# Kernel optimization log

Measured on AMD Instinct MI355X. Metric: run time of the kernel, lower is better.

The kernel has to match this reference:

```python
import jax, jax.numpy as jnp
import numpy as np

LAMB_MAX = 2.0


def cheb_conv_k2(x, edge_index, w0, w1, b):
    """PyG ChebConv with K=2, sym normalization, given lambda_max.
    out = x @ w0 + (L_hat x) @ w1 + b, where
    L_hat = (2/lmax) * (I - D^{-1/2} A D^{-1/2}) - I.
    """
    n = x.shape[0]
    src, dst = edge_index[0], edge_index[1]
    ew = jnp.ones(src.shape, x.dtype)
    deg = jax.ops.segment_sum(ew, src, num_segments=n)
    dinv = jnp.where(deg > 0, jax.lax.rsqrt(jnp.maximum(deg, 1e-12)), 0.0)
    s = 2.0 / LAMB_MAX
    # off-diagonal weights of scaled Laplacian: -s * d_i^{-1/2} d_j^{-1/2}
    norm = (-s) * dinv[src] * dinv[dst]  # [E]
    # gather-scale-scatter: (L_hat x)_offdiag
    agg = jax.ops.segment_sum(norm[:, None] * x[src], dst, num_segments=n)  # [N, F]
    tx1 = (s - 1.0) * x + agg  # diagonal: s*1 (L diag) + (-1) self-loop
    return x @ w0 + tx1 @ w1 + b


def setup_inputs() -> dict:
    key = jax.random.key(0)
    ks = jax.random.split(key, 8)
    N, E, F, H = 100000, 1600000, 128, 128
    x = jax.random.normal(ks[0], (N, F), dtype=jnp.float32)
    edge_index = jax.random.randint(ks[1], (2, E), 0, N, dtype=jnp.int32)
    # glorot-ish init for the two Chebyshev linear weights per layer
    sc1 = (2.0 / (F + H)) ** 0.5
    sc2 = (2.0 / (H + 1)) ** 0.5
    w1_0 = jax.random.normal(ks[2], (F, H), dtype=jnp.float32) * sc1
    w1_1 = jax.random.normal(ks[3], (F, H), dtype=jnp.float32) * sc1
    b1 = jnp.zeros((H,), jnp.float32)
    w2_0 = jax.random.normal(ks[4], (H, 1), dtype=jnp.float32) * sc2
    w2_1 = jax.random.normal(ks[5], (H, 1), dtype=jnp.float32) * sc2
    b2 = jnp.zeros((1,), jnp.float32)
    return {"x": x, "edge_index": edge_index, "w1_0": w1_0, "w1_1": w1_1,
            "b1": b1, "w2_0": w2_0, "w2_1": w2_1, "b2": b2}


def reference(x, edge_index, w1_0, w1_1, b1, w2_0, w2_1, b2):
    h = jax.nn.relu(cheb_conv_k2(x, edge_index, w1_0, w1_1, b1))
    out = jax.nn.sigmoid(cheb_conv_k2(h, edge_index, w2_0, w2_1, b2))
    return out  # [N, 1]
```

## Files before the change

### kernel.cpp

```cpp
#include <hip/hip_runtime.h>
#include <math.h>

#define F 128
#define SCAN_CHUNK 1024
#define CHUNK 32
#define NBLK 128

typedef __attribute__((ext_vector_type(8))) short bf16x8;
typedef __attribute__((ext_vector_type(4))) float f32x4;

__device__ inline unsigned short f2bf(float v) {
  unsigned u = __float_as_uint(v);
  unsigned r = (u + 0x7FFFu + ((u >> 16) & 1u)) >> 16;
  return (unsigned short)r;
}
__device__ inline float bf2f(unsigned short s) {
  return __uint_as_float(((unsigned)s) << 16);
}

__global__ __launch_bounds__(1024) void k_prep2(const int* __restrict__ src,
                                                const int* __restrict__ dst,
                                                const float* __restrict__ x,
                                                unsigned short* __restrict__ xb,
                                                int* __restrict__ cntgD,
                                                int* __restrict__ cntgS, int E,
                                                int NF4, int nb, int per) {
  extern __shared__ int smem[];
  int* cd = smem;
  int* cs = smem + nb;
  int blk = blockIdx.x;
  int tid = threadIdx.x;
  for (int b = tid; b < nb; b += 1024) {
    cd[b] = 0;
    cs[b] = 0;
  }
  __syncthreads();
  int e0 = blk * per;
  int e1 = e0 + per;
  if (e1 > E) e1 = E;
  for (int e = e0 + tid; e < e1; e += 1024) {
    atomicAdd(&cd[dst[e] >> 7], 1);
    atomicAdd(&cs[src[e] >> 7], 1);
  }
  const float4* x4 = (const float4*)x;
  ushort4* xb4 = (ushort4*)xb;
  for (int i = blk * 1024 + tid; i < NF4; i += NBLK * 1024) {
    float4 v = x4[i];
    ushort4 o;
    o.x = f2bf(v.x);
    o.y = f2bf(v.y);
    o.z = f2bf(v.z);
    o.w = f2bf(v.w);
    xb4[i] = o;
  }
  __syncthreads();
  for (int b = tid; b < nb; b += 1024) {
    cntgD[b * NBLK + blk] = cd[b];
    cntgS[b * NBLK + blk] = cs[b];
  }
}

__global__ __launch_bounds__(NBLK) void k_scanBk2(int* __restrict__ cntgD,
                                                  int* __restrict__ cntgS,
                                                  int* __restrict__ totD,
                                                  int* __restrict__ totS, int nb) {
  __shared__ int sh[NBLK];
  int b = blockIdx.x;
  int tid = threadIdx.x;
  int* cntg;
  int* tot;
  int bb;
  if (b < nb) {
    cntg = cntgD;
    tot = totD;
    bb = b;
  } else {
    cntg = cntgS;
    tot = totS;
    bb = b - nb;
  }
  int v = cntg[bb * NBLK + tid];
  int val = v;
  sh[tid] = val;
  __syncthreads();
  for (int off = 1; off < NBLK; off <<= 1) {
    int o = (tid >= off) ? sh[tid - off] : 0;
    __syncthreads();
    val += o;
    sh[tid] = val;
    __syncthreads();
  }
  cntg[bb * NBLK + tid] = val - v;
  if (tid == NBLK - 1) tot[bb] = val;
}

__global__ __launch_bounds__(1024) void k_scanTot(const int* __restrict__ totD,
                                                  const int* __restrict__ totS,
                                                  int* __restrict__ baseD,
                                                  int* __restrict__ baseS, int nb,
                                                  int E) {
  __shared__ int sh[1024];
  int tid = threadIdx.x;
  int v = (tid < nb) ? totD[tid] : 0;
  int val = v;
  sh[tid] = val;
  __syncthreads();
  for (int off = 1; off < 1024; off <<= 1) {
    int o = (tid >= off) ? sh[tid - off] : 0;
    __syncthreads();
    val += o;
    sh[tid] = val;
    __syncthreads();
  }
  if (tid < nb) baseD[tid] = val - v;
  if (tid == 0) baseD[nb] = E;
  __syncthreads();
  v = (tid < nb) ? totS[tid] : 0;
  val = v;
  sh[tid] = val;
  __syncthreads();
  for (int off = 1; off < 1024; off <<= 1) {
    int o = (tid >= off) ? sh[tid - off] : 0;
    __syncthreads();
    val += o;
    sh[tid] = val;
    __syncthreads();
  }
  if (tid < nb) baseS[tid] = val - v;
  if (tid == 0) baseS[nb] = E;
}

__global__ __launch_bounds__(1024) void k_binfill2(
    const int* __restrict__ src, const int* __restrict__ dst,
    const int* __restrict__ cntgD, const int* __restrict__ cntgS,
    const int* __restrict__ baseD, const int* __restrict__ baseS,
    unsigned* __restrict__ binnedD, unsigned char* __restrict__ binnedS, int E,
    int nb, int per) {
  extern __shared__ int smem[];
  int* bD = smem;
  int* cD = smem + nb;
  int* bS = smem + 2 * nb;
  int* cS = smem + 3 * nb;
  int blk = blockIdx.x;
  for (int b = threadIdx.x; b < nb; b += 1024) {
    bD[b] = baseD[b] + cntgD[b * NBLK + blk];
    cD[b] = 0;
    bS[b] = baseS[b] + cntgS[b * NBLK + blk];
    cS[b] = 0;
  }
  __syncthreads();
  int e0 = blk * per;
  int e1 = e0 + per;
  if (e1 > E) e1 = E;
  for (int e = e0 + threadIdx.x; e < e1; e += 1024) {
    int s = src[e];
    int d = dst[e];
    int bk = d >> 7;
    int rk = atomicAdd(&cD[bk], 1);
    binnedD[bD[bk] + rk] = ((unsigned)s << 7) | (unsigned)(d & 127);
    int bs = s >> 7;
    int rs = atomicAdd(&cS[bs], 1);
    binnedS[bS[bs] + rs] = (unsigned char)(s & 127);
  }
}

__global__ __launch_bounds__(256) void k_csr(const unsigned char* __restrict__ binnedS,
                                             const int* __restrict__ baseS,
                                             const unsigned* __restrict__ binnedD,
                                             const int* __restrict__ baseD,
                                             float* __restrict__ dinv,
                                             int* __restrict__ rp,
                                             int* __restrict__ pairs, int N, int E) {
  __shared__ int cnt[128];
  __shared__ int sc[256];
  __shared__ int cur[128];
  int b = blockIdx.x;
  int tid = threadIdx.x;
  int node0 = b << 7;
  if (tid < 128) cnt[tid] = 0;
  __syncthreads();
  int sbeg = baseS[b], send = baseS[b + 1];
  for (int j = sbeg + tid; j < send; j += 256) atomicAdd(&cnt[binnedS[j]], 1);
  __syncthreads();
  if (tid < 128) {
    int node = node0 + tid;
    if (node < N) {
      int c = cnt[tid];
      dinv[node] = c > 0 ? rsqrtf((float)c) : 0.0f;
    }
    cnt[tid] = 0;
  }
  __syncthreads();
  int wbeg = baseD[b], wend = baseD[b + 1];
  for (int j = wbeg + tid; j < wend; j += 256) atomicAdd(&cnt[binnedD[j] & 127u], 1);
  __syncthreads();
  int v = (tid < 128) ? cnt[tid] : 0;
  int val = v;
  sc[tid] = val;
  __syncthreads();
  for (int off = 1; off < 128; off <<= 1) {
    int o = (tid >= off) ? sc[tid - off] : 0;
    __syncthreads();
    val += o;
    sc[tid] = val;
    __syncthreads();
  }
  if (tid < 128) {
    int excl = wbeg + val - v;
    int node = node0 + tid;
    if (node < N) rp[node] = excl;
    cur[tid] = excl;
  }
  if (b == 0 && tid == 0) rp[N] = E;
  __syncthreads();
  for (int j = wbeg + tid; j < wend; j += 256) {
    unsigned e = binnedD[j];
    int idx = atomicAdd(&cur[e & 127u], 1);
    pairs[idx] = (int)(e >> 7);
  }
}

__global__ __launch_bounds__(256) void k_prep(const int* __restrict__ src,
                                              const int* __restrict__ dst,
                                              const float* __restrict__ x,
                                              int* __restrict__ degA,
                                              int* __restrict__ degB,
                                              unsigned short* __restrict__ xb,
                                              int E, int NF4) {
  int t0 = blockIdx.x * 256 + threadIdx.x;
  int stride = gridDim.x * 256;
  for (int i = t0; i < E; i += stride) {
    atomicAdd(&degA[src[i]], 1);
    atomicAdd(&degB[dst[i]], 1);
  }
  const float4* x4 = (const float4*)x;
  ushort4* xb4 = (ushort4*)xb;
  for (int i = t0; i < NF4; i += stride) {
    float4 v = x4[i];
    ushort4 o;
    o.x = f2bf(v.x);
    o.y = f2bf(v.y);
    o.z = f2bf(v.z);
    o.w = f2bf(v.w);
    xb4[i] = o;
  }
}

__global__ __launch_bounds__(256) void k_scanA(const int* __restrict__ deg,
                                               int* __restrict__ rp,
                                               int* __restrict__ bsum, int N) {
  __shared__ int sh[256];
  int tid = threadIdx.x;
  int base = blockIdx.x * SCAN_CHUNK + tid * 4;
  int v0 = 0, v1 = 0, v2 = 0, v3 = 0;
  if (base + 0 < N) v0 = deg[base + 0];
  if (base + 1 < N) v1 = deg[base + 1];
  if (base + 2 < N) v2 = deg[base + 2];
  if (base + 3 < N) v3 = deg[base + 3];
  int ts = v0 + v1 + v2 + v3;
  int val = ts;
  sh[tid] = val;
  __syncthreads();
  for (int off = 1; off < 256; off <<= 1) {
    int other = (tid >= off) ? sh[tid - off] : 0;
    __syncthreads();
    val += other;
    sh[tid] = val;
    __syncthreads();
  }
  int excl = val - ts;
  if (base + 0 < N) rp[base + 0] = excl;
  if (base + 1 < N) rp[base + 1] = excl + v0;
  if (base + 2 < N) rp[base + 2] = excl + v0 + v1;
  if (base + 3 < N) rp[base + 3] = excl + v0 + v1 + v2;
  if (tid == 255) bsum[blockIdx.x] = val;
}

__global__ __launch_bounds__(256) void k_scanB(int* __restrict__ bsum, int nb) {
  __shared__ int sh[256];
  int tid = threadIdx.x;
  int ts = (tid < nb) ? bsum[tid] : 0;
  int val = ts;
  sh[tid] = val;
  __syncthreads();
  for (int off = 1; off < 256; off <<= 1) {
    int other = (tid >= off) ? sh[tid - off] : 0;
    __syncthreads();
    val += other;
    sh[tid] = val;
    __syncthreads();
  }
  if (tid < nb) bsum[tid] = val - ts;
}

__global__ __launch_bounds__(256) void k_scanC(int* __restrict__ rp,
                                               const int* __restrict__ bsum,
                                               int* __restrict__ pos,
                                               const int* __restrict__ degA,
                                               float* __restrict__ dinv, int N,
                                               int E) {
  int i = blockIdx.x * 256 + threadIdx.x;
  if (i < N) {
    int v = rp[i] + bsum[i >> 10];
    rp[i] = v;
    pos[i] = v;
    int d = degA[i];
    dinv[i] = d > 0 ? rsqrtf((float)d) : 0.0f;
  }
  if (i == 0) rp[N] = E;
}

__global__ __launch_bounds__(256) void k_fill(const int* __restrict__ src,
                                              const int* __restrict__ dst,
                                              int* __restrict__ pos,
                                              int* __restrict__ pairs, int E) {
  for (int e = blockIdx.x * 256 + threadIdx.x; e < E; e += gridDim.x * 256) {
    int s = src[e];
    int d = dst[e];
    int idx = atomicAdd(&pos[d], 1);
    pairs[idx] = s;
  }
}

__global__ __launch_bounds__(256) void k_gather1c(
    const int* __restrict__ pairs, const int* __restrict__ rp,
    const unsigned short* __restrict__ xb, const float* __restrict__ dinv,
    unsigned short* __restrict__ tb, int N) {
  int node = (blockIdx.x * 256 + threadIdx.x) >> 5;
  if (node >= N) return;
  int li = threadIdx.x & 31;
  int beg = rp[node], end = rp[node + 1];
  const uint2* x2 = (const uint2*)xb;
  float a0 = 0.f, a1 = 0.f, a2 = 0.f, a3 = 0.f;
  int j = beg;
  for (; j + 3 < end; j += 4) {
    int s0 = pairs[j], s1 = pairs[j + 1], s2 = pairs[j + 2], s3 = pairs[j + 3];
    float w0 = dinv[s0], w1 = dinv[s1], w2 = dinv[s2], w3 = dinv[s3];
    uint2 v0 = x2[(size_t)s0 * 32 + li];
    uint2 v1 = x2[(size_t)s1 * 32 + li];
    uint2 v2 = x2[(size_t)s2 * 32 + li];
    uint2 v3 = x2[(size_t)s3 * 32 + li];
    a0 += w0 * bf2f((unsigned short)v0.x) + w1 * bf2f((unsigned short)v1.x) +
          w2 * bf2f((unsigned short)v2.x) + w3 * bf2f((unsigned short)v3.x);
    a1 += w0 * bf2f((unsigned short)(v0.x >> 16)) +
          w1 * bf2f((unsigned short)(v1.x >> 16)) +
          w2 * bf2f((unsigned short)(v2.x >> 16)) +
          w3 * bf2f((unsigned short)(v3.x >> 16));
    a2 += w0 * bf2f((unsigned short)v0.y) + w1 * bf2f((unsigned short)v1.y) +
          w2 * bf2f((unsigned short)v2.y) + w3 * bf2f((unsigned short)v3.y);
    a3 += w0 * bf2f((unsigned short)(v0.y >> 16)) +
          w1 * bf2f((unsigned short)(v1.y >> 16)) +
          w2 * bf2f((unsigned short)(v2.y >> 16)) +
          w3 * bf2f((unsigned short)(v3.y >> 16));
  }
  for (; j < end; ++j) {
    int s0 = pairs[j];
    float w0 = dinv[s0];
    uint2 v0 = x2[(size_t)s0 * 32 + li];
    a0 += w0 * bf2f((unsigned short)v0.x);
    a1 += w0 * bf2f((unsigned short)(v0.x >> 16));
    a2 += w0 * bf2f((unsigned short)v0.y);
    a3 += w0 * bf2f((unsigned short)(v0.y >> 16));
  }
  float nd = -dinv[node];
  uint2 o;
  o.x = ((unsigned)f2bf(nd * a1) << 16) | f2bf(nd * a0);
  o.y = ((unsigned)f2bf(nd * a3) << 16) | f2bf(nd * a2);
  ((uint2*)tb)[(size_t)node * 32 + li] = o;
}

__global__ __launch_bounds__(256) void k_layer_mfma(
    const unsigned short* __restrict__ xb, const unsigned short* __restrict__ tb,
    const float* __restrict__ dinv, const float* __restrict__ w10,
    const float* __restrict__ w11, const float* __restrict__ b1,
    const float* __restrict__ w20, const float* __restrict__ w21,
    float* __restrict__ p, float* __restrict__ r, int N) {
  __shared__ __align__(16) short Ax[8 * 16 * 40];
  __shared__ __align__(16) short At[8 * 16 * 40];
  __shared__ float p_sh[CHUNK], r_sh[CHUNK];

  const int tid = threadIdx.x;
  const int wave = tid >> 6;
  const int lane = tid & 63;
  const int quad = lane >> 4;
  const int col = lane & 15;

  bf16x8 Bh[2][4][2], Bl[2][4][2];
  float b1f[2], w20f[2], w21f[2];
#pragma unroll
  for (int nt = 0; nt < 2; ++nt) {
    int f = wave * 32 + nt * 16 + col;
    b1f[nt] = b1[f];
    w20f[nt] = w20[f];
    w21f[nt] = w21[f];
  }
#pragma unroll
  for (int mat = 0; mat < 2; ++mat) {
    const float* w = mat ? w11 : w10;
#pragma unroll
    for (int ks = 0; ks < 4; ++ks) {
#pragma unroll
      for (int nt = 0; nt < 2; ++nt) {
        int f = wave * 32 + nt * 16 + col;
        bf16x8 h8, l8;
#pragma unroll
        for (int j = 0; j < 8; ++j) {
          float v = w[(ks * 32 + quad * 8 + j) * F + f];
          unsigned short hi = f2bf(v);
          l8[j] = (short)f2bf(v - bf2f(hi));
          h8[j] = (short)hi;
        }
        Bh[mat][ks][nt] = h8;
        Bl[mat][ks][nt] = l8;
      }
    }
  }

  const int nchunks = (N + CHUNK - 1) / CHUNK;
  for (int chunk = blockIdx.x; chunk < nchunks; chunk += gridDim.x) {
    int node0 = chunk * CHUNK;
    __syncthreads();

    {
      int nloc = tid >> 3;
      int k0 = (tid & 7) * 16;
      int gn = node0 + nloc;
      int mt = nloc >> 4, m = nloc & 15, ks = k0 >> 5, koff = k0 & 31;
      int base = ((mt * 4 + ks) * 16 + m) * 40 + koff;
      const uint2* xr = (const uint2*)(xb + (size_t)gn * F + k0);
      const uint2* tr = (const uint2*)(tb + (size_t)gn * F + k0);
      bool ok = (gn < N);
#pragma unroll
      for (int q4 = 0; q4 < 4; ++q4) {
        uint2 xv = ok ? xr[q4] : make_uint2(0u, 0u);
        uint2 tv = ok ? tr[q4] : make_uint2(0u, 0u);
        *(uint2*)&Ax[base + q4 * 4] = xv;
        *(uint2*)&At[base + q4 * 4] = tv;
      }
      if (tid < CHUNK) {
        p_sh[tid] = 0.f;
        r_sh[tid] = 0.f;
      }
    }
    __syncthreads();

    f32x4 acc[2][2];
#pragma unroll
    for (int mt = 0; mt < 2; ++mt)
#pragma unroll
      for (int nt = 0; nt < 2; ++nt) acc[mt][nt] = (f32x4)0.f;

#pragma unroll
    for (int mt = 0; mt < 2; ++mt) {
#pragma unroll
      for (int ks = 0; ks < 4; ++ks) {
        int ab = ((mt * 4 + ks) * 16 + col) * 40 + quad * 8;
        bf16x8 ax = *(bf16x8*)&Ax[ab];
        bf16x8 at = *(bf16x8*)&At[ab];
#pragma unroll
        for (int nt = 0; nt < 2; ++nt) {
          f32x4 c = acc[mt][nt];
          c = __builtin_amdgcn_mfma_f32_16x16x32_bf16(ax, Bh[0][ks][nt], c, 0, 0, 0);
          c = __builtin_amdgcn_mfma_f32_16x16x32_bf16(ax, Bl[0][ks][nt], c, 0, 0, 0);
          c = __builtin_amdgcn_mfma_f32_16x16x32_bf16(at, Bh[1][ks][nt], c, 0, 0, 0);
          c = __builtin_amdgcn_mfma_f32_16x16x32_bf16(at, Bl[1][ks][nt], c, 0, 0, 0);
          acc[mt][nt] = c;
        }
      }
    }

#pragma unroll
    for (int mt = 0; mt < 2; ++mt) {
      float pp[4], rr[4];
#pragma unroll
      for (int reg = 0; reg < 4; ++reg) {
        float h0 = fmaxf(acc[mt][0][reg] + b1f[0], 0.f);
        float h1 = fmaxf(acc[mt][1][reg] + b1f[1], 0.f);
        pp[reg] = h0 * w20f[0] + h1 * w20f[1];
        rr[reg] = h0 * w21f[0] + h1 * w21f[1];
      }
#pragma unroll
      for (int off = 1; off < 16; off <<= 1) {
#pragma unroll
        for (int reg = 0; reg < 4; ++reg) {
          pp[reg] += __shfl_xor(pp[reg], off);
          rr[reg] += __shfl_xor(rr[reg], off);
        }
      }
      if (col == 0) {
#pragma unroll
        for (int reg = 0; reg < 4; ++reg) {
          atomicAdd(&p_sh[mt * 16 + quad * 4 + reg], pp[reg]);
          atomicAdd(&r_sh[mt * 16 + quad * 4 + reg], rr[reg]);
        }
      }
    }
    __syncthreads();
    if (tid < CHUNK) {
      int gn = node0 + tid;
      if (gn < N) {
        p[gn] = p_sh[tid];
        r[gn] = dinv[gn] * r_sh[tid];
      }
    }
  }
}

__global__ __launch_bounds__(256) void k_gather2_final(
    const int* __restrict__ pairs, const int* __restrict__ rp,
    const float* __restrict__ r2, const float* __restrict__ p,
    const float* __restrict__ dinv, const float* __restrict__ b2,
    float* __restrict__ out, int N) {
  int i = blockIdx.x * 256 + threadIdx.x;
  if (i >= N) return;
  int beg = rp[i], end = rp[i + 1];
  float a = 0.f;
  for (int j = beg; j < end; ++j) a += r2[pairs[j]];
  float z = p[i] - dinv[i] * a + b2[0];
  out[i] = 1.0f / (1.0f + expf(-z));
}

extern "C" void kernel_launch(void* const* d_in, const int* in_sizes, int n_in,
                              void* d_out, int out_size, void* d_ws, size_t ws_size,
                              hipStream_t stream) {
  const float* x = (const float*)d_in[0];
  const int* ei = (const int*)d_in[1];
  const float* w10 = (const float*)d_in[2];
  const float* w11 = (const float*)d_in[3];
  const float* b1 = (const float*)d_in[4];
  const float* w20 = (const float*)d_in[5];
  const float* w21 = (const float*)d_in[6];
  const float* b2 = (const float*)d_in[7];
  float* out = (float*)d_out;
  int N = in_sizes[0] / F;
  int E = in_sizes[1] / 2;
  const int* src = ei;
  const int* dst = ei + E;
  int nbuckets = (N + 127) >> 7;

  size_t off = 0;
  char* base = (char*)d_ws;
  auto take = [&](size_t bytes) {
    void* ptr = base + off;
    off += (bytes + 15) & ~(size_t)15;
    return ptr;
  };
  float* dinv = (float*)take((size_t)N * 4);
  float* p = (float*)take((size_t)N * 4);
  float* r = (float*)take((size_t)N * 4);
  int* rp = (int*)take(((size_t)N + 1) * 4);
  int* degA = (int*)take((size_t)N * 4);
  int* degB = (int*)take((size_t)N * 4);
  int* pos = (int*)take((size_t)N * 4);
  int* bsum = (int*)take(256 * 4);
  int* cntgD = (int*)take((size_t)nbuckets * NBLK * 4);
  int* cntgS = (int*)take((size_t)nbuckets * NBLK * 4);
  int* totD = (int*)take(((size_t)nbuckets + 1) * 4);
  int* totS = (int*)take(((size_t)nbuckets + 1) * 4);
  int* baseD = (int*)take(((size_t)nbuckets + 1) * 4);
  int* baseS = (int*)take(((size_t)nbuckets + 1) * 4);
  int* pairs = (int*)take((size_t)E * 4);
  unsigned short* xb = (unsigned short*)take((size_t)N * F * 2);
  unsigned short* tb = (unsigned short*)take((size_t)N * F * 2);
  if (off > ws_size) return;
  unsigned* binnedD = (unsigned*)tb;
  unsigned char* binnedS = (unsigned char*)tb + (((size_t)E * 4 + 255) & ~(size_t)255);

  int NF4 = N * (F / 4);
  int per = (E + NBLK - 1) / NBLK;

  if (nbuckets <= 1024 && (size_t)E * 5 + 256 <= (size_t)N * F * 2) {
    k_prep2<<<NBLK, 1024, (size_t)nbuckets * 8, stream>>>(src, dst, x, xb, cntgD,
                                                          cntgS, E, NF4, nbuckets,
                                                          per);
    k_scanBk2<<<2 * nbuckets, NBLK, 0, stream>>>(cntgD, cntgS, totD, totS, nbuckets);
    k_scanTot<<<1, 1024, 0, stream>>>(totD, totS, baseD, baseS, nbuckets, E);
    k_binfill2<<<NBLK, 1024, (size_t)nbuckets * 16, stream>>>(
        src, dst, cntgD, cntgS, baseD, baseS, binnedD, binnedS, E, nbuckets, per);
    k_csr<<<nbuckets, 256, 0, stream>>>(binnedS, baseS, binnedD, baseD, dinv, rp,
                                        pairs, N, E);
  } else {
    int nb_scan = (N + SCAN_CHUNK - 1) / SCAN_CHUNK;
    hipMemsetAsync(degA, 0, 2 * (size_t)N * sizeof(int), stream);
    k_prep<<<2048, 256, 0, stream>>>(src, dst, x, degA, degB, xb, E, NF4);
    k_scanA<<<nb_scan, 256, 0, stream>>>(degB, rp, bsum, N);
    k_scanB<<<1, 256, 0, stream>>>(bsum, nb_scan);
    k_scanC<<<(N + 255) / 256, 256, 0, stream>>>(rp, bsum, pos, degA, dinv, N, E);
    k_fill<<<2048, 256, 0, stream>>>(src, dst, pos, pairs, E);
  }
  k_gather1c<<<(N + 7) / 8, 256, 0, stream>>>(pairs, rp, xb, dinv, tb, N);
  k_layer_mfma<<<512, 256, 0, stream>>>(xb, tb, dinv, w10, w11, b1, w20, w21, p, r,
                                        N);
  k_gather2_final<<<(N + 255) / 256, 256, 0, stream>>>(pairs, rp, r, p, dinv, b2,
                                                       out, N);
}
```

Baseline: 313.3 us.

## Fuse layer-1 gather into MFMA layer kernel and drop split-bf16 weight terms

The neighbor gather-aggregate now runs inside the MFMA layer kernel and writes straight into shared memory, so the bf16 intermediate tb no longer round-trips through global memory. The grid becomes one block per 32-node chunk instead of a persistent loop. The weights are also reduced from a hi+lo bf16 split to a single bf16 term, which halves the MFMA count but lowers weight precision. Per-block setup, including loading and converting the weights into registers, is now repeated for each of about 3125 blocks, and the binned scratch buffers get their own workspace space.

```diff
diff --git a/kernel.cpp b/kernel.cpp
--- a/kernel.cpp
+++ b/kernel.cpp
@@ -322,59 +322,13 @@
   }
 }
 
-__global__ __launch_bounds__(256) void k_gather1c(
+__global__ __launch_bounds__(256) void k_fused(
     const int* __restrict__ pairs, const int* __restrict__ rp,
     const unsigned short* __restrict__ xb, const float* __restrict__ dinv,
-    unsigned short* __restrict__ tb, int N) {
-  int node = (blockIdx.x * 256 + threadIdx.x) >> 5;
-  if (node >= N) return;
-  int li = threadIdx.x & 31;
-  int beg = rp[node], end = rp[node + 1];
-  const uint2* x2 = (const uint2*)xb;
-  float a0 = 0.f, a1 = 0.f, a2 = 0.f, a3 = 0.f;
-  int j = beg;
-  for (; j + 3 < end; j += 4) {
-    int s0 = pairs[j], s1 = pairs[j + 1], s2 = pairs[j + 2], s3 = pairs[j + 3];
-    float w0 = dinv[s0], w1 = dinv[s1], w2 = dinv[s2], w3 = dinv[s3];
-    uint2 v0 = x2[(size_t)s0 * 32 + li];
-    uint2 v1 = x2[(size_t)s1 * 32 + li];
-    uint2 v2 = x2[(size_t)s2 * 32 + li];
-    uint2 v3 = x2[(size_t)s3 * 32 + li];
-    a0 += w0 * bf2f((unsigned short)v0.x) + w1 * bf2f((unsigned short)v1.x) +
-          w2 * bf2f((unsigned short)v2.x) + w3 * bf2f((unsigned short)v3.x);
-    a1 += w0 * bf2f((unsigned short)(v0.x >> 16)) +
-          w1 * bf2f((unsigned short)(v1.x >> 16)) +
-          w2 * bf2f((unsigned short)(v2.x >> 16)) +
-          w3 * bf2f((unsigned short)(v3.x >> 16));
-    a2 += w0 * bf2f((unsigned short)v0.y) + w1 * bf2f((unsigned short)v1.y) +
-          w2 * bf2f((unsigned short)v2.y) + w3 * bf2f((unsigned short)v3.y);
-    a3 += w0 * bf2f((unsigned short)(v0.y >> 16)) +
-          w1 * bf2f((unsigned short)(v1.y >> 16)) +
-          w2 * bf2f((unsigned short)(v2.y >> 16)) +
-          w3 * bf2f((unsigned short)(v3.y >> 16));
-  }
-  for (; j < end; ++j) {
-    int s0 = pairs[j];
-    float w0 = dinv[s0];
-    uint2 v0 = x2[(size_t)s0 * 32 + li];
-    a0 += w0 * bf2f((unsigned short)v0.x);
-    a1 += w0 * bf2f((unsigned short)(v0.x >> 16));
-    a2 += w0 * bf2f((unsigned short)v0.y);
-    a3 += w0 * bf2f((unsigned short)(v0.y >> 16));
-  }
-  float nd = -dinv[node];
-  uint2 o;
-  o.x = ((unsigned)f2bf(nd * a1) << 16) | f2bf(nd * a0);
-  o.y = ((unsigned)f2bf(nd * a3) << 16) | f2bf(nd * a2);
-  ((uint2*)tb)[(size_t)node * 32 + li] = o;
-}
-
-__global__ __launch_bounds__(256) void k_layer_mfma(
-    const unsigned short* __restrict__ xb, const unsigned short* __restrict__ tb,
-    const float* __restrict__ dinv, const float* __restrict__ w10,
-    const float* __restrict__ w11, const float* __restrict__ b1,
-    const float* __restrict__ w20, const float* __restrict__ w21,
-    float* __restrict__ p, float* __restrict__ r, int N) {
+    const float* __restrict__ w10, const float* __restrict__ w11,
+    const float* __restrict__ b1, const float* __restrict__ w20,
+    const float* __restrict__ w21, float* __restrict__ p, float* __restrict__ r,
+    int N) {
   __shared__ __align__(16) short Ax[8 * 16 * 40];
   __shared__ __align__(16) short At[8 * 16 * 40];
   __shared__ float p_sh[CHUNK], r_sh[CHUNK];
@@ -385,7 +339,7 @@
   const int quad = lane >> 4;
   const int col = lane & 15;
 
-  bf16x8 Bh[2][4][2], Bl[2][4][2];
+  bf16x8 B0[4][2], B1[4][2];
   float b1f[2], w20f[2], w21f[2];
 #pragma unroll
   for (int nt = 0; nt < 2; ++nt) {
@@ -395,113 +349,154 @@
     w21f[nt] = w21[f];
   }
 #pragma unroll
-  for (int mat = 0; mat < 2; ++mat) {
-    const float* w = mat ? w11 : w10;
+  for (int ks = 0; ks < 4; ++ks) {
+#pragma unroll
+    for (int nt = 0; nt < 2; ++nt) {
+      int f = wave * 32 + nt * 16 + col;
+      bf16x8 h0, h1;
+#pragma unroll
+      for (int j = 0; j < 8; ++j) {
+        h0[j] = (short)f2bf(w10[(ks * 32 + quad * 8 + j) * F + f]);
+        h1[j] = (short)f2bf(w11[(ks * 32 + quad * 8 + j) * F + f]);
+      }
+      B0[ks][nt] = h0;
+      B1[ks][nt] = h1;
+    }
+  }
+
+  int node0 = blockIdx.x * CHUNK;
+
+  {
+    int nloc = tid >> 3;
+    int k0 = (tid & 7) * 16;
+    int gn = node0 + nloc;
+    int mt = nloc >> 4, m = nloc & 15, ks = k0 >> 5, koff = k0 & 31;
+    int base = ((mt * 4 + ks) * 16 + m) * 40 + koff;
+    const uint2* xr = (const uint2*)(xb + (size_t)gn * F + k0);
+    bool ok = (gn < N);
+#pragma unroll
+    for (int q4 = 0; q4 < 4; ++q4) {
+      uint2 xv = ok ? xr[q4] : make_uint2(0u, 0u);
+      *(uint2*)&Ax[base + q4 * 4] = xv;
+    }
+    if (tid < CHUNK) {
+      p_sh[tid] = 0.f;
+      r_sh[tid] = 0.f;
+    }
+  }
+
+  {
+    int hw = tid >> 5;
+    int li = tid & 31;
+    const uint2* x2 = (const uint2*)xb;
+    int ks = li >> 3, koff = (li & 7) * 4;
+#pragma unroll 1
+    for (int nn = 0; nn < 4; ++nn) {
+      int nloc = hw * 4 + nn;
+      int gn = node0 + nloc;
+      float a0 = 0.f, a1 = 0.f, a2 = 0.f, a3 = 0.f;
+      float nd = 0.f;
+      if (gn < N) {
+        int beg = rp[gn], end = rp[gn + 1];
+        int j = beg;
+        for (; j + 3 < end; j += 4) {
+          int s0 = pairs[j], s1 = pairs[j + 1], s2 = pairs[j + 2], s3 = pairs[j + 3];
+          float w0 = dinv[s0], w1 = dinv[s1], w2 = dinv[s2], w3 = dinv[s3];
+          uint2 v0 = x2[(size_t)s0 * 32 + li];
+          uint2 v1 = x2[(size_t)s1 * 32 + li];
+          uint2 v2 = x2[(size_t)s2 * 32 + li];
+          uint2 v3 = x2[(size_t)s3 * 32 + li];
+          a0 += w0 * bf2f((unsigned short)v0.x) + w1 * bf2f((unsigned short)v1.x) +
+                w2 * bf2f((unsigned short)v2.x) + w3 * bf2f((unsigned short)v3.x);
+          a1 += w0 * bf2f((unsigned short)(v0.x >> 16)) +
+                w1 * bf2f((unsigned short)(v1.x >> 16)) +
+                w2 * bf2f((unsigned short)(v2.x >> 16)) +
+                w3 * bf2f((unsigned short)(v3.x >> 16));
+          a2 += w0 * bf2f((unsigned short)v0.y) + w1 * bf2f((unsigned short)v1.y) +
+                w2 * bf2f((unsigned short)v2.y) + w3 * bf2f((unsigned short)v3.y);
+          a3 += w0 * bf2f((unsigned short)(v0.y >> 16)) +
+                w1 * bf2f((unsigned short)(v1.y >> 16)) +
+                w2 * bf2f((unsigned short)(v2.y >> 16)) +
+                w3 * bf2f((unsigned short)(v3.y >> 16));
+        }
+        for (; j < end; ++j) {
+          int s0 = pairs[j];
+          float w0 = dinv[s0];
+          uint2 v0 = x2[(size_t)s0 * 32 + li];
+          a0 += w0 * bf2f((unsigned short)v0.x);
+          a1 += w0 * bf2f((unsigned short)(v0.x >> 16));
+          a2 += w0 * bf2f((unsigned short)v0.y);
+          a3 += w0 * bf2f((unsigned short)(v0.y >> 16));
+        }
+        nd = -dinv[gn];
+      }
+      int mt = nloc >> 4, m = nloc & 15;
+      int base = ((mt * 4 + ks) * 16 + m) * 40 + koff;
+      short4 o;
+      o.x = (short)f2bf(nd * a0);
+      o.y = (short)f2bf(nd * a1);
+      o.z = (short)f2bf(nd * a2);
+      o.w = (short)f2bf(nd * a3);
+      *(short4*)&At[base] = o;
+    }
+  }
+  __syncthreads();
+
+  f32x4 acc[2][2];
+#pragma unroll
+  for (int mt = 0; mt < 2; ++mt)
+#pragma unroll
+    for (int nt = 0; nt < 2; ++nt) acc[mt][nt] = (f32x4)0.f;
+
+#pragma unroll
+  for (int mt = 0; mt < 2; ++mt) {
 #pragma unroll
     for (int ks = 0; ks < 4; ++ks) {
+      int ab = ((mt * 4 + ks) * 16 + col) * 40 + quad * 8;
+      bf16x8 ax = *(bf16x8*)&Ax[ab];
+      bf16x8 at = *(bf16x8*)&At[ab];
 #pragma unroll
       for (int nt = 0; nt < 2; ++nt) {
-        int f = wave * 32 + nt * 16 + col;
-        bf16x8 h8, l8;
-#pragma unroll
-        for (int j = 0; j < 8; ++j) {
-          float v = w[(ks * 32 + quad * 8 + j) * F + f];
-          unsigned short hi = f2bf(v);
-          l8[j] = (short)f2bf(v - bf2f(hi));
-          h8[j] = (short)hi;
-        }
-        Bh[mat][ks][nt] = h8;
-        Bl[mat][ks][nt] = l8;
+        f32x4 c = acc[mt][nt];
+        c = __builtin_amdgcn_mfma_f32_16x16x32_bf16(ax, B0[ks][nt], c, 0, 0, 0);
+        c = __builtin_amdgcn_mfma_f32_16x16x32_bf16(at, B1[ks][nt], c, 0, 0, 0);
+        acc[mt][nt] = c;
       }
     }
   }
 
-  const int nchunks = (N + CHUNK - 1) / CHUNK;
-  for (int chunk = blockIdx.x; chunk < nchunks; chunk += gridDim.x) {
-    int node0 = chunk * CHUNK;
-    __syncthreads();
-
-    {
-      int nloc = tid >> 3;
-      int k0 = (tid & 7) * 16;
-      int gn = node0 + nloc;
-      int mt = nloc >> 4, m = nloc & 15, ks = k0 >> 5, koff = k0 & 31;
-      int base = ((mt * 4 + ks) * 16 + m) * 40 + koff;
-      const uint2* xr = (const uint2*)(xb + (size_t)gn * F + k0);
-      const uint2* tr = (const uint2*)(tb + (size_t)gn * F + k0);
-      bool ok = (gn < N);
-#pragma unroll
-      for (int q4 = 0; q4 < 4; ++q4) {
-        uint2 xv = ok ? xr[q4] : make_uint2(0u, 0u);
-        uint2 tv = ok ? tr[q4] : make_uint2(0u, 0u);
-        *(uint2*)&Ax[base + q4 * 4] = xv;
-        *(uint2*)&At[base + q4 * 4] = tv;
+#pragma unroll
+  for (int mt = 0; mt < 2; ++mt) {
+    float pp[4], rr[4];
+#pragma unroll
+    for (int reg = 0; reg < 4; ++reg) {
+      float h0 = fmaxf(acc[mt][0][reg] + b1f[0], 0.f);
+      float h1 = fmaxf(acc[mt][1][reg] + b1f[1], 0.f);
+      pp[reg] = h0 * w20f[0] + h1 * w20f[1];
+      rr[reg] = h0 * w21f[0] + h1 * w21f[1];
+    }
+#pragma unroll
+    for (int off = 1; off < 16; off <<= 1) {
+#pragma unroll
+      for (int reg = 0; reg < 4; ++reg) {
+        pp[reg] += __shfl_xor(pp[reg], off);
+        rr[reg] += __shfl_xor(rr[reg], off);
       }
-      if (tid < CHUNK) {
-        p_sh[tid] = 0.f;
-        r_sh[tid] = 0.f;
+    }
+    if (col == 0) {
+#pragma unroll
+      for (int reg = 0; reg < 4; ++reg) {
+        atomicAdd(&p_sh[mt * 16 + quad * 4 + reg], pp[reg]);
+        atomicAdd(&r_sh[mt * 16 + quad * 4 + reg], rr[reg]);
       }
     }
-    __syncthreads();
-
-    f32x4 acc[2][2];
-#pragma unroll
-    for (int mt = 0; mt < 2; ++mt)
-#pragma unroll
-      for (int nt = 0; nt < 2; ++nt) acc[mt][nt] = (f32x4)0.f;
-
-#pragma unroll
-    for (int mt = 0; mt < 2; ++mt) {
-#pragma unroll
-      for (int ks = 0; ks < 4; ++ks) {
-        int ab = ((mt * 4 + ks) * 16 + col) * 40 + quad * 8;
-        bf16x8 ax = *(bf16x8*)&Ax[ab];
-        bf16x8 at = *(bf16x8*)&At[ab];
-#pragma unroll
-        for (int nt = 0; nt < 2; ++nt) {
-          f32x4 c = acc[mt][nt];
-          c = __builtin_amdgcn_mfma_f32_16x16x32_bf16(ax, Bh[0][ks][nt], c, 0, 0, 0);
-          c = __builtin_amdgcn_mfma_f32_16x16x32_bf16(ax, Bl[0][ks][nt], c, 0, 0, 0);
-          c = __builtin_amdgcn_mfma_f32_16x16x32_bf16(at, Bh[1][ks][nt], c, 0, 0, 0);
-          c = __builtin_amdgcn_mfma_f32_16x16x32_bf16(at, Bl[1][ks][nt], c, 0, 0, 0);
-          acc[mt][nt] = c;
-        }
-      }
-    }
-
-#pragma unroll
-    for (int mt = 0; mt < 2; ++mt) {
-      float pp[4], rr[4];
-#pragma unroll
-      for (int reg = 0; reg < 4; ++reg) {
-        float h0 = fmaxf(acc[mt][0][reg] + b1f[0], 0.f);
-        float h1 = fmaxf(acc[mt][1][reg] + b1f[1], 0.f);
-        pp[reg] = h0 * w20f[0] + h1 * w20f[1];
-        rr[reg] = h0 * w21f[0] + h1 * w21f[1];
-      }
-#pragma unroll
-      for (int off = 1; off < 16; off <<= 1) {
-#pragma unroll
-        for (int reg = 0; reg < 4; ++reg) {
-          pp[reg] += __shfl_xor(pp[reg], off);
-          rr[reg] += __shfl_xor(rr[reg], off);
-        }
-      }
-      if (col == 0) {
-#pragma unroll
-        for (int reg = 0; reg < 4; ++reg) {
-          atomicAdd(&p_sh[mt * 16 + quad * 4 + reg], pp[reg]);
-          atomicAdd(&r_sh[mt * 16 + quad * 4 + reg], rr[reg]);
-        }
-      }
-    }
-    __syncthreads();
-    if (tid < CHUNK) {
-      int gn = node0 + tid;
-      if (gn < N) {
-        p[gn] = p_sh[tid];
-        r[gn] = dinv[gn] * r_sh[tid];
-      }
+  }
+  __syncthreads();
+  if (tid < CHUNK) {
+    int gn = node0 + tid;
+    if (gn < N) {
+      p[gn] = p_sh[tid];
+      r[gn] = dinv[gn] * r_sh[tid];
     }
   }
 }
@@ -560,16 +555,15 @@
   int* baseD = (int*)take(((size_t)nbuckets + 1) * 4);
   int* baseS = (int*)take(((size_t)nbuckets + 1) * 4);
   int* pairs = (int*)take((size_t)E * 4);
+  unsigned* binnedD = (unsigned*)take((size_t)E * 4);
+  unsigned char* binnedS = (unsigned char*)take((size_t)E);
   unsigned short* xb = (unsigned short*)take((size_t)N * F * 2);
-  unsigned short* tb = (unsigned short*)take((size_t)N * F * 2);
   if (off > ws_size) return;
-  unsigned* binnedD = (unsigned*)tb;
-  unsigned char* binnedS = (unsigned char*)tb + (((size_t)E * 4 + 255) & ~(size_t)255);
 
   int NF4 = N * (F / 4);
   int per = (E + NBLK - 1) / NBLK;
 
-  if (nbuckets <= 1024 && (size_t)E * 5 + 256 <= (size_t)N * F * 2) {
+  if (nbuckets <= 1024) {
     k_prep2<<<NBLK, 1024, (size_t)nbuckets * 8, stream>>>(src, dst, x, xb, cntgD,
                                                           cntgS, E, NF4, nbuckets,
                                                           per);
@@ -588,9 +582,8 @@
     k_scanC<<<(N + 255) / 256, 256, 0, stream>>>(rp, bsum, pos, degA, dinv, N, E);
     k_fill<<<2048, 256, 0, stream>>>(src, dst, pos, pairs, E);
   }
-  k_gather1c<<<(N + 7) / 8, 256, 0, stream>>>(pairs, rp, xb, dinv, tb, N);
-  k_layer_mfma<<<512, 256, 0, stream>>>(xb, tb, dinv, w10, w11, b1, w20, w21, p, r,
-                                        N);
+  k_fused<<<(N + CHUNK - 1) / CHUNK, 256, 0, stream>>>(pairs, rp, xb, dinv, w10,
+                                                       w11, b1, w20, w21, p, r, N);
   k_gather2_final<<<(N + 255) / 256, 256, 0, stream>>>(pairs, rp, r, p, dinv, b2,
                                                        out, N);
 }
```

Result: slower. 392.0 us (+25.1%).
